# Performance work log

Measured on AMD Instinct MI355X. Metric: run time of the kernel, lower is better.

The kernel has to match this reference:

```python
import jax, jax.numpy as jnp
import numpy as np

B, N, DIM = 1, 100_000, 512
HEADS, DIM_HEAD, M = 8, 64, 64


def setup_inputs() -> dict:
    key = jax.random.key(0)
    ks = jax.random.split(key, 9)
    s = 0.04  # ~ kaiming-ish scale for dim=512
    return {
        "x": jax.random.normal(ks[0], (B, N, DIM), dtype=jnp.float32),
        "temperature": jnp.full((1, HEADS, 1, 1), 0.5, dtype=jnp.float32),
        "w_slice": jax.random.normal(ks[1], (HEADS * M, DIM), dtype=jnp.float32) * s,
        "b_slice": jnp.zeros((HEADS * M,), dtype=jnp.float32),
        "w1": jax.random.normal(ks[2], (DIM_HEAD, DIM), dtype=jnp.float32) * s,
        "b1": jnp.zeros((DIM_HEAD,), dtype=jnp.float32),
        "wq": jax.random.normal(ks[3], (DIM_HEAD, DIM_HEAD), dtype=jnp.float32) * 0.125,
        "wk": jax.random.normal(ks[4], (DIM_HEAD, DIM_HEAD), dtype=jnp.float32) * 0.125,
        "wv": jax.random.normal(ks[5], (DIM_HEAD, DIM_HEAD), dtype=jnp.float32) * 0.125,
        "w3": jax.random.normal(ks[6], (DIM_HEAD, DIM_HEAD), dtype=jnp.float32) * 0.125,
        "b3": jnp.zeros((DIM_HEAD,), dtype=jnp.float32),
    }


def reference(x, temperature, w_slice, b_slice, w1, b1, wq, wk, wv, w3, b3):
    b, n, c = x.shape
    # slice logits: (B,N,H*M) -> (B,H,N,M)
    logits = jnp.einsum("bnc,ec->bne", x, w_slice) + b_slice
    logits = logits.reshape(b, n, HEADS, M).transpose(0, 2, 1, 3)
    temp = jnp.clip(temperature, 0.1, 5.0)
    w = jax.nn.softmax(logits / temp, axis=-1)          # (B,H,N,M)
    d = w.sum(axis=2)                                    # (B,H,M)
    # N -> M aggregation (w^T @ x per head)
    s_raw = jnp.einsum("bhnm,bnc->bhmc", w, x)          # (B,H,M,C)
    s = jnp.einsum("bhmc,dc->bhmd", s_raw / (d[..., None] + 1e-5), w1) + b1  # (B,H,M,dh)
    q = jnp.einsum("bhmd,ed->bhme", s, wq)
    k = jnp.einsum("bhmd,ed->bhme", s, wk)
    v = jnp.einsum("bhmd,ed->bhme", s, wv)
    scale = 1.0 / jnp.sqrt(jnp.asarray(DIM_HEAD, dtype=s.dtype))
    attn = jax.nn.softmax(jnp.einsum("bhme,bhle->bhml", q, k) * scale, axis=-1)
    s_att = jnp.einsum("bhml,bhle->bhme", attn, v)      # (B,H,M,dh)
    s_out = jnp.einsum("bhme,de->bhmd", s_att, w3) + b3
    # deslice: w @ s_out -> (B,H,N,dh) -> (B,N,H*dh)
    x_out = jnp.einsum("bhnm,bhmd->bhnd", w, s_out)
    return x_out.transpose(0, 2, 1, 3).reshape(b, n, HEADS * DIM_HEAD)
```

## Files before the change

kernel.cpp:

```cpp
#include <hip/hip_runtime.h>

typedef _Float16 f16;
typedef _Float16 f16x8 __attribute__((ext_vector_type(8)));
typedef _Float16 f16x4 __attribute__((ext_vector_type(4)));
typedef float    f32x4 __attribute__((ext_vector_type(4)));

#define N_TOK   100000
#define NPAD    100032
#define NT1     1563
#define CDIM    512
#define KSTEPS  (NPAD/32)
#define K2SPL   128

#define O_WT     ((size_t)0)
#define SZ_WT    ((size_t)512*NPAD*2)
#define O_YT     (O_WT + SZ_WT)
#define SZ_YT    ((size_t)64*NPAD*2)
#define O_WFR    (O_YT + SZ_YT)
#define SZ_WFR   ((size_t)16*4*9*64*8*2)
#define O_SPP    (O_WFR + SZ_WFR)
#define SZ_SPP   ((size_t)K2SPL*32768*4)
#define O_DPP    (O_SPP + SZ_SPP)
#define SZ_DPP   ((size_t)K2SPL*512*4)
#define O_SPRE   (O_DPP + SZ_DPP)
#define SZ_SPRE  ((size_t)32768*4)
#define O_DSTD   (O_SPRE + SZ_SPRE)
#define SZ_DSTD  ((size_t)512*4)
#define O_SOUT   (O_DSTD + SZ_DSTD)
#define SZ_SOUT  ((size_t)8*64*64*2)

__global__ void k0_pack(const float* __restrict__ wsf, const float* __restrict__ w1f,
                        f16* __restrict__ wfr) {
    int c = blockIdx.x * 256 + threadIdx.x;
    int lane = c & 63, g = c >> 6;
    int u  = g % 9,  r = g / 9;
    int we = r & 3,  kg = r >> 2;
    int col = lane & 15, quad = lane >> 4;
    int k = kg * 32 + quad * 8;
    const float* src;
    if (u < 8) src = wsf + (size_t)(we*128 + u*16 + col) * CDIM + k;
    else       src = w1f + (size_t)(we*16  + col) * CDIM + k;
    float4 a = *(const float4*)(src);
    float4 b = *(const float4*)(src + 4);
    f16x8 h;
    h[0]=(f16)a.x; h[1]=(f16)a.y; h[2]=(f16)a.z; h[3]=(f16)a.w;
    h[4]=(f16)b.x; h[5]=(f16)b.y; h[6]=(f16)b.z; h[7]=(f16)b.w;
    *(f16x8*)(wfr + (size_t)c * 8) = h;
}

#define XROW 40
#define TPITCH 72
__launch_bounds__(256, 2)
__global__ void k1_slice(const float* __restrict__ x, const float* __restrict__ temperature,
                         const f16* __restrict__ wfr, const float* __restrict__ bsl,
                         f16* __restrict__ wT, f16* __restrict__ yT) {
    __shared__ f16 smem[512 * TPITCH];
    f16* lX = smem;
    f16* lT = smem;

    const int tid  = threadIdx.x;
    const int wave = tid >> 6;
    const int lane = tid & 63;
    const int quad = lane >> 4;
    const int col  = lane & 15;
    const int n0   = blockIdx.x * 64;

    const int srow = tid >> 2, sch = tid & 3;
    int snr = n0 + srow; if (snr > N_TOK - 1) snr = N_TOK - 1;
    const float* sbase = x + (size_t)snr * CDIM + sch * 8;

    {
        float4 a = *(const float4*)(sbase);
        float4 b = *(const float4*)(sbase + 4);
        f16x8 h;
        h[0]=(f16)a.x; h[1]=(f16)a.y; h[2]=(f16)a.z; h[3]=(f16)a.w;
        h[4]=(f16)b.x; h[5]=(f16)b.y; h[6]=(f16)b.z; h[7]=(f16)b.w;
        *(f16x8*)(&lX[srow * XROW + sch * 8]) = h;
    }

    f32x4 acc[4][9];
    #pragma unroll
    for (int nf = 0; nf < 4; ++nf)
        #pragma unroll
        for (int u = 0; u < 9; ++u) acc[nf][u] = f32x4{0.f,0.f,0.f,0.f};

    __syncthreads();

    #pragma unroll 2
    for (int kg = 0; kg < 16; ++kg) {
        const f16* wb = wfr + ((size_t)(kg*4 + wave) * 9) * 512 + (size_t)lane * 8;
        f16x8 bf[9];
        #pragma unroll
        for (int u = 0; u < 9; ++u) bf[u] = *(const f16x8*)(wb + u * 512);

        float4 xa, xb;
        if (kg < 15) {
            xa = *(const float4*)(sbase + (kg + 1) * 32);
            xb = *(const float4*)(sbase + (kg + 1) * 32 + 4);
        }

        const f16* xbuf = lX + (kg & 1) * (64 * XROW);
        f16x8 af[4];
        #pragma unroll
        for (int nf = 0; nf < 4; ++nf)
            af[nf] = *(const f16x8*)(xbuf + (nf*16 + col) * XROW + quad * 8);

        #pragma unroll
        for (int nf = 0; nf < 4; ++nf)
            #pragma unroll
            for (int u = 0; u < 9; ++u)
                acc[nf][u] = __builtin_amdgcn_mfma_f32_16x16x32_f16(af[nf], bf[u], acc[nf][u], 0, 0, 0);

        if (kg < 15) {
            f16x8 h;
            h[0]=(f16)xa.x; h[1]=(f16)xa.y; h[2]=(f16)xa.z; h[3]=(f16)xa.w;
            h[4]=(f16)xb.x; h[5]=(f16)xb.y; h[6]=(f16)xb.z; h[7]=(f16)xb.w;
            *(f16x8*)(&lX[((kg + 1) & 1) * (64 * XROW) + srow * XROW + sch * 8]) = h;
        }
        __syncthreads();
    }

    #pragma unroll
    for (int u = 0; u < 8; ++u) {
        float b = bsl[wave*128 + u*16 + col];
        #pragma unroll
        for (int nf = 0; nf < 4; ++nf)
            #pragma unroll
            for (int r = 0; r < 4; ++r) acc[nf][u][r] += b;
    }
    float invt[2];
    #pragma unroll
    for (int hh = 0; hh < 2; ++hh) {
        float tv = temperature[wave*2 + hh];
        tv = fminf(fmaxf(tv, 0.1f), 5.0f);
        invt[hh] = 1.0f / tv;
    }

    #pragma unroll
    for (int nf = 0; nf < 4; ++nf) {
        const int nloc = nf*16 + quad*4;
        #pragma unroll
        for (int hh = 0; hh < 2; ++hh) {
            float mx[4];
            #pragma unroll
            for (int r = 0; r < 4; ++r) {
                float m01 = fmaxf(acc[nf][hh*4+0][r], acc[nf][hh*4+1][r]);
                float m23 = fmaxf(acc[nf][hh*4+2][r], acc[nf][hh*4+3][r]);
                mx[r] = fmaxf(m01, m23);
            }
            #pragma unroll
            for (int d = 1; d < 16; d <<= 1)
                #pragma unroll
                for (int r = 0; r < 4; ++r) mx[r] = fmaxf(mx[r], __shfl_xor(mx[r], d));
            float sm[4] = {0.f, 0.f, 0.f, 0.f};
            #pragma unroll
            for (int uu = 0; uu < 4; ++uu)
                #pragma unroll
                for (int r = 0; r < 4; ++r) {
                    float ev = __expf((acc[nf][hh*4+uu][r] - mx[r]) * invt[hh]);
                    acc[nf][hh*4+uu][r] = ev;
                    sm[r] += ev;
                }
            #pragma unroll
            for (int d = 1; d < 16; d <<= 1)
                #pragma unroll
                for (int r = 0; r < 4; ++r) sm[r] += __shfl_xor(sm[r], d);
            #pragma unroll
            for (int r = 0; r < 4; ++r) sm[r] = 1.0f / sm[r];
            #pragma unroll
            for (int uu = 0; uu < 4; ++uu) {
                f16x4 pk;
                #pragma unroll
                for (int r = 0; r < 4; ++r) {
                    int n = n0 + nloc + r;
                    float wv = (n < N_TOK) ? acc[nf][hh*4+uu][r] * sm[r] : 0.0f;
                    pk[r] = (f16)wv;
                }
                int e = wave*128 + (hh*4 + uu)*16 + col;
                *(f16x4*)(lT + (size_t)e*TPITCH + nloc) = pk;
            }
        }
        {
            f16x4 pk;
            #pragma unroll
            for (int r = 0; r < 4; ++r) {
                int n = n0 + nloc + r;
                pk[r] = (n < N_TOK) ? (f16)acc[nf][8][r] : (f16)0.f;
            }
            *(f16x4*)(yT + (size_t)(wave*16 + col) * NPAD + n0 + nloc) = pk;
        }
    }
    __syncthreads();

    #pragma unroll
    for (int i = 0; i < 16; ++i) {
        int id = tid + i*256;
        int e = id >> 3, p = id & 7;
        f16x8 v = *(const f16x8*)(lT + (size_t)e*TPITCH + p*8);
        *(f16x8*)(wT + (size_t)e*NPAD + n0 + p*8) = v;
    }
}

#define K2_LOAD(AF, BF, kss)                                                         \
    {   int nb_ = (kss)*32 + quad*8;                                                 \
        _Pragma("unroll")                                                            \
        for (int v = 0; v < 4; ++v)                                                  \
            BF[v] = *(const f16x8*)(yT + (size_t)(v*16 + col)*NPAD + nb_);           \
        _Pragma("unroll")                                                            \
        for (int u = 0; u < 2; ++u)                                                  \
            AF[u] = *(const f16x8*)(wT + (size_t)(ebase + u*16 + col)*NPAD + nb_);   \
    }
#define K2_MFMA(AF, BF)                                                              \
    {   _Pragma("unroll")                                                            \
        for (int u = 0; u < 2; ++u) {                                                \
            _Pragma("unroll")                                                        \
            for (int v = 0; v < 4; ++v)                                              \
                acc[u][v] = __builtin_amdgcn_mfma_f32_16x16x32_f16(AF[u], BF[v], acc[u][v], 0, 0, 0); \
            float s_ = 0.f;                                                          \
            _Pragma("unroll")                                                        \
            for (int j = 0; j < 8; ++j) s_ += (float)AF[u][j];                       \
            dac[u] += s_;                                                            \
        }                                                                            \
    }
__launch_bounds__(256, 4)
__global__ void k2_spre(const f16* __restrict__ wT, const f16* __restrict__ yT,
                        float* __restrict__ spp, float* __restrict__ dpp) {
    const int tid = threadIdx.x, wave = tid >> 6, lane = tid & 63;
    const int quad = lane >> 4, col = lane & 15;
    const int slot = blockIdx.x >> 2, equad = blockIdx.x & 3;
    const int ebase = equad * 128 + wave * 32;

    const int ks0 = (slot * KSTEPS) >> 7;
    const int ks1 = ((slot + 1) * KSTEPS) >> 7;

    f32x4 acc[2][4];
    float dac[2];
    #pragma unroll
    for (int u = 0; u < 2; ++u) {
        dac[u] = 0.f;
        #pragma unroll
        for (int v = 0; v < 4; ++v) acc[u][v] = f32x4{0.f,0.f,0.f,0.f};
    }

    f16x8 afA[2], bfA[4], afB[2], bfB[4];
    K2_LOAD(afA, bfA, ks0)
    int ks = ks0;
    for (; ks + 2 <= ks1; ks += 2) {
        K2_LOAD(afB, bfB, ks + 1)
        K2_MFMA(afA, bfA)
        K2_LOAD(afA, bfA, ks + 2)
        K2_MFMA(afB, bfB)
    }
    if (ks < ks1) K2_MFMA(afA, bfA)

    #pragma unroll
    for (int u = 0; u < 2; ++u) {
        dac[u] += __shfl_xor(dac[u], 16);
        dac[u] += __shfl_xor(dac[u], 32);
    }
    if (quad == 0) {
        #pragma unroll
        for (int u = 0; u < 2; ++u)
            dpp[slot*512 + ebase + u*16 + col] = dac[u];
    }
    float* dst = spp + (size_t)slot * 32768 + (size_t)equad * 8192;
    #pragma unroll
    for (int u = 0; u < 2; ++u)
        #pragma unroll
        for (int v = 0; v < 4; ++v)
            *(f32x4*)(dst + (size_t)((wave*2 + u)*4 + v)*256 + (size_t)lane*4) = acc[u][v];
}

__global__ void k2r_reduce(const float* __restrict__ spp, const float* __restrict__ dpp,
                           float* __restrict__ spre, float* __restrict__ dstd) {
    int i = blockIdx.x*256 + threadIdx.x;
    float s = 0.f;
    for (int p = 0; p < K2SPL; ++p) s += spp[(size_t)p*32768 + i];
    int r = i & 3, L = (i >> 2) & 63, v = (i >> 8) & 3, g = (i >> 10) & 7, eq = (i >> 13) & 3;
    int e = eq*128 + (g >> 1)*32 + (g & 1)*16 + (L >> 4)*4 + r;
    int d = v*16 + (L & 15);
    spre[e*64 + d] = s;
    if (i < 512) {
        float tt = 0.f;
        for (int p = 0; p < K2SPL; ++p) tt += dpp[p*512 + i];
        dstd[i] = tt;
    }
}

__global__ void k3_attn(const float* __restrict__ spre, const float* __restrict__ dstd,
                        const float* __restrict__ b1, const float* __restrict__ wq,
                        const float* __restrict__ wk, const float* __restrict__ wv,
                        const float* __restrict__ w3, const float* __restrict__ b3,
                        f16* __restrict__ sout) {
    __shared__ float wa[64][65], wb[64][65], wc[64][65];
    __shared__ float ss[64][65], qq[64][65], kk[64][65], vv[64][65], sc[64][65];
    const int h = blockIdx.x, tid = threadIdx.x;

    for (int i = tid; i < 4096; i += 256) {
        int r = i >> 6, c = i & 63;
        wa[r][c] = wq[i];
        wb[r][c] = wk[i];
        wc[r][c] = wv[i];
        ss[r][c] = spre[h*4096 + i] / (dstd[h*64 + r] + 1e-5f) + b1[c];
    }
    __syncthreads();

    #pragma unroll
    for (int it = 0; it < 16; ++it) {
        int m = it*4 + (tid >> 6), e = tid & 63;
        float aq = 0.f, ak = 0.f, av = 0.f;
        #pragma unroll 8
        for (int d = 0; d < 64; ++d) {
            float sv = ss[m][d];
            aq += sv * wa[e][d];
            ak += sv * wb[e][d];
            av += sv * wc[e][d];
        }
        qq[m][e] = aq; kk[m][e] = ak; vv[m][e] = av;
    }
    __syncthreads();

    for (int i = tid; i < 4096; i += 256) wa[i >> 6][i & 63] = w3[i];
    #pragma unroll
    for (int it = 0; it < 16; ++it) {
        int m = it*4 + (tid >> 6), l = tid & 63;
        float a = 0.f;
        #pragma unroll 8
        for (int e = 0; e < 64; ++e) a += qq[m][e] * kk[l][e];
        sc[m][l] = a * 0.125f;
    }
    __syncthreads();

    if (tid < 64) {
        int m = tid;
        float mx = -1e30f;
        #pragma unroll 8
        for (int l = 0; l < 64; ++l) mx = fmaxf(mx, sc[m][l]);
        float sm = 0.f;
        #pragma unroll 8
        for (int l = 0; l < 64; ++l) { float ev = __expf(sc[m][l] - mx); sc[m][l] = ev; sm += ev; }
        float rs = 1.0f / sm;
        #pragma unroll 8
        for (int l = 0; l < 64; ++l) sc[m][l] *= rs;
    }
    __syncthreads();

    #pragma unroll
    for (int it = 0; it < 16; ++it) {
        int m = it*4 + (tid >> 6), e = tid & 63;
        float a = 0.f;
        #pragma unroll 8
        for (int l = 0; l < 64; ++l) a += sc[m][l] * vv[l][e];
        ss[m][e] = a;
    }
    __syncthreads();

    #pragma unroll
    for (int it = 0; it < 16; ++it) {
        int d = it*4 + (tid >> 6), m = tid & 63;
        float a = b3[d];
        #pragma unroll 8
        for (int e = 0; e < 64; ++e) a += ss[m][e] * wa[d][e];
        sout[(h*64 + d)*64 + m] = (f16)a;
    }
}

#define K4PITCH 36
__launch_bounds__(256, 4)
__global__ void k4_deslice(const f16* __restrict__ wT, const f16* __restrict__ sout,
                           float* __restrict__ out) {
    __shared__ f16 ldsW[512 * K4PITCH];
    const int tid = threadIdx.x, wave = tid >> 6, lane = tid & 63;
    const int quad = lane >> 4, col = lane & 15;
    const int n0 = blockIdx.x * 32;

    #pragma unroll
    for (int i = 0; i < 8; ++i) {
        int id = tid + i*256;
        int e = id >> 2, p = id & 3;
        f16x8 v = *(const f16x8*)(wT + (size_t)e*NPAD + n0 + p*8);
        *(f16x8*)(ldsW + (size_t)e*K4PITCH + p*8) = v;
    }
    __syncthreads();

    f32x4 acc[2][2][4];
    #pragma unroll
    for (int hh = 0; hh < 2; ++hh)
        #pragma unroll
        for (int t = 0; t < 2; ++t)
            #pragma unroll
            for (int v = 0; v < 4; ++v) acc[hh][t][v] = f32x4{0.f,0.f,0.f,0.f};

    #pragma unroll
    for (int hh = 0; hh < 2; ++hh) {
        int h = wave*2 + hh;
        #pragma unroll
        for (int ks = 0; ks < 2; ++ks) {
            f16x8 af[2], bf[4];
            #pragma unroll
            for (int t = 0; t < 2; ++t) {
                f16x8 a;
                #pragma unroll
                for (int j = 0; j < 8; ++j)
                    a[j] = ldsW[(size_t)(h*64 + ks*32 + quad*8 + j)*K4PITCH + t*16 + col];
                af[t] = a;
            }
            #pragma unroll
            for (int v = 0; v < 4; ++v)
                bf[v] = *(const f16x8*)(sout + (size_t)(h*64 + v*16 + col)*64 + ks*32 + quad*8);
            #pragma unroll
            for (int t = 0; t < 2; ++t)
                #pragma unroll
                for (int v = 0; v < 4; ++v)
                    acc[hh][t][v] = __builtin_amdgcn_mfma_f32_16x16x32_f16(af[t], bf[v], acc[hh][t][v], 0, 0, 0);
        }
    }

    #pragma unroll
    for (int hh = 0; hh < 2; ++hh) {
        int h = wave*2 + hh;
        #pragma unroll
        for (int t = 0; t < 2; ++t)
            #pragma unroll
            for (int v = 0; v < 4; ++v)
                #pragma unroll
                for (int r = 0; r < 4; ++r) {
                    int n = n0 + t*16 + quad*4 + r;
                    if (n < N_TOK)
                        out[(size_t)n*512 + h*64 + v*16 + col] = acc[hh][t][v][r];
                }
    }
}

extern "C" void kernel_launch(void* const* d_in, const int* in_sizes, int n_in,
                              void* d_out, int out_size, void* d_ws, size_t ws_size,
                              hipStream_t stream) {
    const float* x           = (const float*)d_in[0];
    const float* temperature = (const float*)d_in[1];
    const float* w_slice     = (const float*)d_in[2];
    const float* b_slice     = (const float*)d_in[3];
    const float* w1          = (const float*)d_in[4];
    const float* b1          = (const float*)d_in[5];
    const float* wq          = (const float*)d_in[6];
    const float* wk          = (const float*)d_in[7];
    const float* wv          = (const float*)d_in[8];
    const float* w3          = (const float*)d_in[9];
    const float* b3          = (const float*)d_in[10];
    float* out = (float*)d_out;
    char*  ws  = (char*)d_ws;

    f16*   wT    = (f16*)(ws + O_WT);
    f16*   yT    = (f16*)(ws + O_YT);
    f16*   wfr   = (f16*)(ws + O_WFR);
    float* spp   = (float*)(ws + O_SPP);
    float* dpp   = (float*)(ws + O_DPP);
    float* spre  = (float*)(ws + O_SPRE);
    float* dstd  = (float*)(ws + O_DSTD);
    f16*   sout  = (f16*)(ws + O_SOUT);

    k0_pack<<<144, 256, 0, stream>>>(w_slice, w1, wfr);
    k1_slice<<<NT1, 256, 0, stream>>>(x, temperature, wfr, b_slice, wT, yT);
    k2_spre<<<K2SPL*4, 256, 0, stream>>>(wT, yT, spp, dpp);
    k2r_reduce<<<128, 256, 0, stream>>>(spp, dpp, spre, dstd);
    k3_attn<<<8, 256, 0, stream>>>(spre, dstd, b1, wq, wk, wv, w3, b3, sout);
    k4_deslice<<<KSTEPS, 256, 0, stream>>>(wT, sout, out);
}
```

Before: 598.7 us.

## Split slice kernel by head group, split attention rows, swizzle deslice blocks per XCD

k1_slice now launches two blocks per 64-token tile, each handling four heads. This halves the accumulator registers and LDS and allows three blocks per CU, at the cost of loading and converting x twice. Only the first head group computes the y projection. k3_attn is split across 4 query-row quarters per head (32 blocks instead of 8), so the K/V projections are recomputed in each block. k4_deslice remaps block IDs so that each XCD gets a contiguous token range.

```diff
diff --git a/kernel.cpp b/kernel.cpp
--- a/kernel.cpp
+++ b/kernel.cpp
@@ -50,11 +50,11 @@
 
 #define XROW 40
 #define TPITCH 72
-__launch_bounds__(256, 2)
+__launch_bounds__(256, 3)
 __global__ void k1_slice(const float* __restrict__ x, const float* __restrict__ temperature,
                          const f16* __restrict__ wfr, const float* __restrict__ bsl,
                          f16* __restrict__ wT, f16* __restrict__ yT) {
-    __shared__ f16 smem[512 * TPITCH];
+    __shared__ f16 smem[256 * TPITCH];
     f16* lX = smem;
     f16* lT = smem;
 
@@ -63,7 +63,9 @@
     const int lane = tid & 63;
     const int quad = lane >> 4;
     const int col  = lane & 15;
-    const int n0   = blockIdx.x * 64;
+    const int hgrp = blockIdx.x & 1;
+    const int n0   = (blockIdx.x >> 1) * 64;
+    const int h    = hgrp * 4 + wave;
 
     const int srow = tid >> 2, sch = tid & 3;
     int snr = n0 + srow; if (snr > N_TOK - 1) snr = N_TOK - 1;
@@ -72,26 +74,30 @@
     {
         float4 a = *(const float4*)(sbase);
         float4 b = *(const float4*)(sbase + 4);
-        f16x8 h;
-        h[0]=(f16)a.x; h[1]=(f16)a.y; h[2]=(f16)a.z; h[3]=(f16)a.w;
-        h[4]=(f16)b.x; h[5]=(f16)b.y; h[6]=(f16)b.z; h[7]=(f16)b.w;
-        *(f16x8*)(&lX[srow * XROW + sch * 8]) = h;
-    }
-
-    f32x4 acc[4][9];
+        f16x8 hh;
+        hh[0]=(f16)a.x; hh[1]=(f16)a.y; hh[2]=(f16)a.z; hh[3]=(f16)a.w;
+        hh[4]=(f16)b.x; hh[5]=(f16)b.y; hh[6]=(f16)b.z; hh[7]=(f16)b.w;
+        *(f16x8*)(&lX[srow * XROW + sch * 8]) = hh;
+    }
+
+    f32x4 acc[4][5];
     #pragma unroll
     for (int nf = 0; nf < 4; ++nf)
         #pragma unroll
-        for (int u = 0; u < 9; ++u) acc[nf][u] = f32x4{0.f,0.f,0.f,0.f};
+        for (int u = 0; u < 5; ++u) acc[nf][u] = f32x4{0.f,0.f,0.f,0.f};
 
     __syncthreads();
 
     #pragma unroll 2
     for (int kg = 0; kg < 16; ++kg) {
-        const f16* wb = wfr + ((size_t)(kg*4 + wave) * 9) * 512 + (size_t)lane * 8;
-        f16x8 bf[9];
-        #pragma unroll
-        for (int u = 0; u < 9; ++u) bf[u] = *(const f16x8*)(wb + u * 512);
+        const f16* wb = wfr + ((size_t)(kg*4 + (h >> 1)) * 9 + (size_t)(h & 1) * 4) * 512
+                            + (size_t)lane * 8;
+        f16x8 bf[4];
+        #pragma unroll
+        for (int j = 0; j < 4; ++j) bf[j] = *(const f16x8*)(wb + j * 512);
+        f16x8 bfy;
+        if (hgrp == 0)
+            bfy = *(const f16x8*)(wfr + ((size_t)(kg*4 + wave) * 9 + 8) * 512 + (size_t)lane * 8);
 
         float4 xa, xb;
         if (kg < 15) {
@@ -108,84 +114,82 @@
         #pragma unroll
         for (int nf = 0; nf < 4; ++nf)
             #pragma unroll
-            for (int u = 0; u < 9; ++u)
-                acc[nf][u] = __builtin_amdgcn_mfma_f32_16x16x32_f16(af[nf], bf[u], acc[nf][u], 0, 0, 0);
+            for (int j = 0; j < 4; ++j)
+                acc[nf][j] = __builtin_amdgcn_mfma_f32_16x16x32_f16(af[nf], bf[j], acc[nf][j], 0, 0, 0);
+        if (hgrp == 0) {
+            #pragma unroll
+            for (int nf = 0; nf < 4; ++nf)
+                acc[nf][4] = __builtin_amdgcn_mfma_f32_16x16x32_f16(af[nf], bfy, acc[nf][4], 0, 0, 0);
+        }
 
         if (kg < 15) {
-            f16x8 h;
-            h[0]=(f16)xa.x; h[1]=(f16)xa.y; h[2]=(f16)xa.z; h[3]=(f16)xa.w;
-            h[4]=(f16)xb.x; h[5]=(f16)xb.y; h[6]=(f16)xb.z; h[7]=(f16)xb.w;
-            *(f16x8*)(&lX[((kg + 1) & 1) * (64 * XROW) + srow * XROW + sch * 8]) = h;
+            f16x8 hh;
+            hh[0]=(f16)xa.x; hh[1]=(f16)xa.y; hh[2]=(f16)xa.z; hh[3]=(f16)xa.w;
+            hh[4]=(f16)xb.x; hh[5]=(f16)xb.y; hh[6]=(f16)xb.z; hh[7]=(f16)xb.w;
+            *(f16x8*)(&lX[((kg + 1) & 1) * (64 * XROW) + srow * XROW + sch * 8]) = hh;
         }
         __syncthreads();
     }
 
     #pragma unroll
-    for (int u = 0; u < 8; ++u) {
-        float b = bsl[wave*128 + u*16 + col];
+    for (int j = 0; j < 4; ++j) {
+        float b = bsl[h*64 + j*16 + col];
         #pragma unroll
         for (int nf = 0; nf < 4; ++nf)
             #pragma unroll
-            for (int r = 0; r < 4; ++r) acc[nf][u][r] += b;
-    }
-    float invt[2];
-    #pragma unroll
-    for (int hh = 0; hh < 2; ++hh) {
-        float tv = temperature[wave*2 + hh];
-        tv = fminf(fmaxf(tv, 0.1f), 5.0f);
-        invt[hh] = 1.0f / tv;
-    }
+            for (int r = 0; r < 4; ++r) acc[nf][j][r] += b;
+    }
+    float tv = temperature[h];
+    tv = fminf(fmaxf(tv, 0.1f), 5.0f);
+    const float invt = 1.0f / tv;
 
     #pragma unroll
     for (int nf = 0; nf < 4; ++nf) {
         const int nloc = nf*16 + quad*4;
-        #pragma unroll
-        for (int hh = 0; hh < 2; ++hh) {
-            float mx[4];
+        float mx[4];
+        #pragma unroll
+        for (int r = 0; r < 4; ++r) {
+            float m01 = fmaxf(acc[nf][0][r], acc[nf][1][r]);
+            float m23 = fmaxf(acc[nf][2][r], acc[nf][3][r]);
+            mx[r] = fmaxf(m01, m23);
+        }
+        #pragma unroll
+        for (int d = 1; d < 16; d <<= 1)
+            #pragma unroll
+            for (int r = 0; r < 4; ++r) mx[r] = fmaxf(mx[r], __shfl_xor(mx[r], d));
+        float sm[4] = {0.f, 0.f, 0.f, 0.f};
+        #pragma unroll
+        for (int j = 0; j < 4; ++j)
             #pragma unroll
             for (int r = 0; r < 4; ++r) {
-                float m01 = fmaxf(acc[nf][hh*4+0][r], acc[nf][hh*4+1][r]);
-                float m23 = fmaxf(acc[nf][hh*4+2][r], acc[nf][hh*4+3][r]);
-                mx[r] = fmaxf(m01, m23);
+                float ev = __expf((acc[nf][j][r] - mx[r]) * invt);
+                acc[nf][j][r] = ev;
+                sm[r] += ev;
             }
-            #pragma unroll
-            for (int d = 1; d < 16; d <<= 1)
-                #pragma unroll
-                for (int r = 0; r < 4; ++r) mx[r] = fmaxf(mx[r], __shfl_xor(mx[r], d));
-            float sm[4] = {0.f, 0.f, 0.f, 0.f};
-            #pragma unroll
-            for (int uu = 0; uu < 4; ++uu)
-                #pragma unroll
-                for (int r = 0; r < 4; ++r) {
-                    float ev = __expf((acc[nf][hh*4+uu][r] - mx[r]) * invt[hh]);
-                    acc[nf][hh*4+uu][r] = ev;
-                    sm[r] += ev;
-                }
-            #pragma unroll
-            for (int d = 1; d < 16; d <<= 1)
-                #pragma unroll
-                for (int r = 0; r < 4; ++r) sm[r] += __shfl_xor(sm[r], d);
-            #pragma unroll
-            for (int r = 0; r < 4; ++r) sm[r] = 1.0f / sm[r];
-            #pragma unroll
-            for (int uu = 0; uu < 4; ++uu) {
-                f16x4 pk;
-                #pragma unroll
-                for (int r = 0; r < 4; ++r) {
-                    int n = n0 + nloc + r;
-                    float wv = (n < N_TOK) ? acc[nf][hh*4+uu][r] * sm[r] : 0.0f;
-                    pk[r] = (f16)wv;
-                }
-                int e = wave*128 + (hh*4 + uu)*16 + col;
-                *(f16x4*)(lT + (size_t)e*TPITCH + nloc) = pk;
-            }
-        }
-        {
+        #pragma unroll
+        for (int d = 1; d < 16; d <<= 1)
+            #pragma unroll
+            for (int r = 0; r < 4; ++r) sm[r] += __shfl_xor(sm[r], d);
+        #pragma unroll
+        for (int r = 0; r < 4; ++r) sm[r] = 1.0f / sm[r];
+        #pragma unroll
+        for (int j = 0; j < 4; ++j) {
             f16x4 pk;
             #pragma unroll
             for (int r = 0; r < 4; ++r) {
                 int n = n0 + nloc + r;
-                pk[r] = (n < N_TOK) ? (f16)acc[nf][8][r] : (f16)0.f;
+                float wv = (n < N_TOK) ? acc[nf][j][r] * sm[r] : 0.0f;
+                pk[r] = (f16)wv;
+            }
+            int e_loc = wave*64 + j*16 + col;
+            *(f16x4*)(lT + (size_t)e_loc*TPITCH + nloc) = pk;
+        }
+        if (hgrp == 0) {
+            f16x4 pk;
+            #pragma unroll
+            for (int r = 0; r < 4; ++r) {
+                int n = n0 + nloc + r;
+                pk[r] = (n < N_TOK) ? (f16)acc[nf][4][r] : (f16)0.f;
             }
             *(f16x4*)(yT + (size_t)(wave*16 + col) * NPAD + n0 + nloc) = pk;
         }
@@ -193,11 +197,11 @@
     __syncthreads();
 
     #pragma unroll
-    for (int i = 0; i < 16; ++i) {
+    for (int i = 0; i < 8; ++i) {
         int id = tid + i*256;
         int e = id >> 3, p = id & 7;
         f16x8 v = *(const f16x8*)(lT + (size_t)e*TPITCH + p*8);
-        *(f16x8*)(wT + (size_t)e*NPAD + n0 + p*8) = v;
+        *(f16x8*)(wT + (size_t)(hgrp*256 + e)*NPAD + n0 + p*8) = v;
     }
 }
 
@@ -293,8 +297,9 @@
                         const float* __restrict__ w3, const float* __restrict__ b3,
                         f16* __restrict__ sout) {
     __shared__ float wa[64][65], wb[64][65], wc[64][65];
-    __shared__ float ss[64][65], qq[64][65], kk[64][65], vv[64][65], sc[64][65];
-    const int h = blockIdx.x, tid = threadIdx.x;
+    __shared__ float ss[64][65], kk[64][65], vv[64][65];
+    __shared__ float qq[16][65], sc[16][65];
+    const int h = blockIdx.x >> 2, ms = blockIdx.x & 3, tid = threadIdx.x;
 
     for (int i = tid; i < 4096; i += 256) {
         int r = i >> 6, c = i & 63;
@@ -308,60 +313,67 @@
     #pragma unroll
     for (int it = 0; it < 16; ++it) {
         int m = it*4 + (tid >> 6), e = tid & 63;
-        float aq = 0.f, ak = 0.f, av = 0.f;
+        float ak = 0.f, av = 0.f;
         #pragma unroll 8
         for (int d = 0; d < 64; ++d) {
             float sv = ss[m][d];
-            aq += sv * wa[e][d];
             ak += sv * wb[e][d];
             av += sv * wc[e][d];
         }
-        qq[m][e] = aq; kk[m][e] = ak; vv[m][e] = av;
+        kk[m][e] = ak; vv[m][e] = av;
+    }
+    #pragma unroll
+    for (int it = 0; it < 4; ++it) {
+        int ml = it*4 + (tid >> 6), e = tid & 63;
+        float aq = 0.f;
+        #pragma unroll 8
+        for (int d = 0; d < 64; ++d) aq += ss[ms*16 + ml][d] * wa[e][d];
+        qq[ml][e] = aq;
     }
     __syncthreads();
 
     for (int i = tid; i < 4096; i += 256) wa[i >> 6][i & 63] = w3[i];
     #pragma unroll
-    for (int it = 0; it < 16; ++it) {
-        int m = it*4 + (tid >> 6), l = tid & 63;
+    for (int it = 0; it < 4; ++it) {
+        int ml = it*4 + (tid >> 6), l = tid & 63;
         float a = 0.f;
         #pragma unroll 8
-        for (int e = 0; e < 64; ++e) a += qq[m][e] * kk[l][e];
-        sc[m][l] = a * 0.125f;
-    }
-    __syncthreads();
-
-    if (tid < 64) {
-        int m = tid;
+        for (int e = 0; e < 64; ++e) a += qq[ml][e] * kk[l][e];
+        sc[ml][l] = a * 0.125f;
+    }
+    __syncthreads();
+
+    if (tid < 16) {
+        int ml = tid;
         float mx = -1e30f;
         #pragma unroll 8
-        for (int l = 0; l < 64; ++l) mx = fmaxf(mx, sc[m][l]);
+        for (int l = 0; l < 64; ++l) mx = fmaxf(mx, sc[ml][l]);
         float sm = 0.f;
         #pragma unroll 8
-        for (int l = 0; l < 64; ++l) { float ev = __expf(sc[m][l] - mx); sc[m][l] = ev; sm += ev; }
+        for (int l = 0; l < 64; ++l) { float ev = __expf(sc[ml][l] - mx); sc[ml][l] = ev; sm += ev; }
         float rs = 1.0f / sm;
         #pragma unroll 8
-        for (int l = 0; l < 64; ++l) sc[m][l] *= rs;
-    }
-    __syncthreads();
-
-    #pragma unroll
-    for (int it = 0; it < 16; ++it) {
-        int m = it*4 + (tid >> 6), e = tid & 63;
+        for (int l = 0; l < 64; ++l) sc[ml][l] *= rs;
+    }
+    __syncthreads();
+
+    #pragma unroll
+    for (int it = 0; it < 4; ++it) {
+        int ml = it*4 + (tid >> 6), e = tid & 63;
         float a = 0.f;
         #pragma unroll 8
-        for (int l = 0; l < 64; ++l) a += sc[m][l] * vv[l][e];
-        ss[m][e] = a;
-    }
-    __syncthreads();
-
-    #pragma unroll
-    for (int it = 0; it < 16; ++it) {
-        int d = it*4 + (tid >> 6), m = tid & 63;
+        for (int l = 0; l < 64; ++l) a += sc[ml][l] * vv[l][e];
+        qq[ml][e] = a;
+    }
+    __syncthreads();
+
+    #pragma unroll
+    for (int it = 0; it < 4; ++it) {
+        int d = it*16 + (tid >> 4), ml = tid & 15;
         float a = b3[d];
         #pragma unroll 8
-        for (int e = 0; e < 64; ++e) a += ss[m][e] * wa[d][e];
-        sout[(h*64 + d)*64 + m] = (f16)a;
+        for (int e = 0; e < 64; ++e) a += qq[ml][e] * wa[d][e];
+        sout[(h*64 + d)*64 + ms*16 + ml] = (f16)a;
     }
 }
 
@@ -372,7 +384,12 @@
     __shared__ f16 ldsW[512 * K4PITCH];
     const int tid = threadIdx.x, wave = tid >> 6, lane = tid & 63;
     const int quad = lane >> 4, col = lane & 15;
-    const int n0 = blockIdx.x * 32;
+
+    const int bid = blockIdx.x;
+    const int xcd = bid & 7, idx = bid >> 3;
+    const int q = KSTEPS >> 3, r = KSTEPS & 7;
+    const int swz = (xcd < r ? xcd*(q+1) : r*(q+1) + (xcd - r)*q) + idx;
+    const int n0 = swz * 32;
 
     #pragma unroll
     for (int i = 0; i < 8; ++i) {
@@ -424,10 +441,10 @@
             #pragma unroll
             for (int v = 0; v < 4; ++v)
                 #pragma unroll
-                for (int r = 0; r < 4; ++r) {
-                    int n = n0 + t*16 + quad*4 + r;
+                for (int r2 = 0; r2 < 4; ++r2) {
+                    int n = n0 + t*16 + quad*4 + r2;
                     if (n < N_TOK)
-                        out[(size_t)n*512 + h*64 + v*16 + col] = acc[hh][t][v][r];
+                        out[(size_t)n*512 + h*64 + v*16 + col] = acc[hh][t][v][r2];
                 }
     }
 }
@@ -459,9 +476,9 @@
     f16*   sout  = (f16*)(ws + O_SOUT);
 
     k0_pack<<<144, 256, 0, stream>>>(w_slice, w1, wfr);
-    k1_slice<<<NT1, 256, 0, stream>>>(x, temperature, wfr, b_slice, wT, yT);
+    k1_slice<<<NT1*2, 256, 0, stream>>>(x, temperature, wfr, b_slice, wT, yT);
     k2_spre<<<K2SPL*4, 256, 0, stream>>>(wT, yT, spp, dpp);
     k2r_reduce<<<128, 256, 0, stream>>>(spp, dpp, spre, dstd);
-    k3_attn<<<8, 256, 0, stream>>>(spre, dstd, b1, wq, wk, wv, w3, b3, sout);
+    k3_attn<<<32, 256, 0, stream>>>(spre, dstd, b1, wq, wk, wv, w3, b3, sout);
     k4_deslice<<<KSTEPS, 256, 0, stream>>>(wT, sout, out);
 }
```

Result: faster. 579.7 us (-3.2%).
